# Kernel optimization log

Hardware: AMD Instinct MI355X
Metric: run time of the kernel (lower is better)

Reference implementation:

```python
import jax, jax.numpy as jnp
import numpy as np

DELTA = 0.1  # fixed Gaussian temperature from __init__


def setup_inputs() -> dict:
    key = jax.random.key(0)
    k1, k2 = jax.random.split(key)
    B, T_TEXT, C = 16, 1024, 512
    T_FEAT = 4096  # static upper bound on sum(durations) per row (durations < 5 -> max 4*1024)
    x = jax.random.normal(k1, (B, T_TEXT, C), dtype=jnp.float32)
    durations = jax.random.randint(k2, (B, T_TEXT), 0, 5, dtype=jnp.int32)
    text_mask = jnp.ones((B, T_TEXT), dtype=bool)  # seqs_layout: valid text positions
    return {"x": x, "durations": durations, "text_mask": text_mask, "t_feat": T_FEAT}


def reference(x, durations, text_mask, t_feat):
    # x: (B, T_text, C); durations: (B, T_text) int; text_mask: (B, T_text) bool
    dtype = x.dtype
    d = durations.astype(dtype)
    out_lens = d.sum(axis=1)                                   # (B,)
    t = jnp.arange(t_feat, dtype=dtype)[None, :]               # (1, T_feat)
    y_mask = t < out_lens[:, None]                             # (B, T_feat) valid frames
    t = t * y_mask.astype(dtype)                               # zero out padded frames
    c = jnp.cumsum(d, axis=-1) - d * 0.5                       # (B, T_text) token centers
    # Gaussian energy over (frame, token) pairs: (B, T_feat, T_text)
    energy = -DELTA * (t[:, :, None] - c[:, None, :]) ** 2
    energy = jnp.where(text_mask[:, None, :], energy, -jnp.inf)
    p_attn = jax.nn.softmax(energy, axis=2)                    # softmax over T_text
    y = jnp.einsum("bft,btc->bfc", p_attn, x)                  # (B, T_feat, C)
    return y, out_lens.astype(jnp.int32)
```

## Files before the change

kernel.cpp:

```cpp
#include <hip/hip_runtime.h>
#include <stdint.h>


#define T_TEXT 1024
#define NEGK -0.14426950408889634f
#define CUT 6.5f
#define WIN2F 49.0f

typedef float vfloat4 __attribute__((ext_vector_type(4)));

__device__ __forceinline__ void nt_store4(float* p, float4 v) {
    vfloat4 nv;
    nv.x = v.x; nv.y = v.y; nv.z = v.z; nv.w = v.w;
    __builtin_nontemporal_store(nv, (vfloat4*)p);
}

#define FMA_GROUP(W4, XV)                                                    \
    {                                                                        \
        const float4 w4 = W4;                                                \
        const float ws = (w4.x + w4.y) + (w4.z + w4.w);                      \
        if (ws != 0.f) {                                                     \
            acc[f].x += w4.x * XV[0].x; acc[f].y += w4.x * XV[0].y;          \
            acc[f].z += w4.x * XV[0].z; acc[f].w += w4.x * XV[0].w;          \
            acc[f].x += w4.y * XV[1].x; acc[f].y += w4.y * XV[1].y;          \
            acc[f].z += w4.y * XV[1].z; acc[f].w += w4.y * XV[1].w;          \
            acc[f].x += w4.z * XV[2].x; acc[f].y += w4.z * XV[2].y;          \
            acc[f].z += w4.z * XV[2].z; acc[f].w += w4.z * XV[2].w;          \
            acc[f].x += w4.w * XV[3].x; acc[f].y += w4.w * XV[3].y;          \
            acc[f].z += w4.w * XV[3].z; acc[f].w += w4.w * XV[3].w;          \
            den[f] += ws;                                                    \
        }                                                                    \
    }

__global__ __launch_bounds__(256, 4) void gauss_kernel(const float* __restrict__ x,
                                                       const int* __restrict__ dur,
                                                       float* __restrict__ y,
                                                       float* __restrict__ out_lens_f,
                                                       int F) {
    const int C = 512;
    int bid = blockIdx.x;
    const int nwg = gridDim.x;
    if ((nwg & 7) == 0) bid = (bid & 7) * (nwg >> 3) + (bid >> 3);
    const int nt = F >> 4;
    const int b = bid / nt;
    const int f0 = (bid - b * nt) << 4;
    const int tid = threadIdx.x;
    const int lane = tid & 63, wid = tid >> 6;
    const int fg = tid >> 7;
    const int chb = (tid & 127) << 2;

    __shared__ float clds[T_TEXT];
    __shared__ float wlds[16][64];
    __shared__ int wtot[4];
    __shared__ int wred[4];

    const int4 d4 = ((const int4*)(dur + b * T_TEXT))[tid];
    const int p0 = d4.x, p1 = p0 + d4.y, p2 = p1 + d4.z, p3 = p2 + d4.w;
    int s = p3;
#pragma unroll
    for (int off = 1; off < 64; off <<= 1) {
        int n = __shfl_up(s, off);
        if (lane >= off) s += n;
    }
    if (lane == 63) wtot[wid] = s;
    __syncthreads();
    int base = s - p3;
    const int w0 = wtot[0], w1 = wtot[1], w2 = wtot[2], w3 = wtot[3];
    const int out_len = (w0 + w1) + (w2 + w3);
    if (wid > 0) base += w0;
    if (wid > 1) base += w1;
    if (wid > 2) base += w2;
    float4 cv;
    cv.x = (float)(base + p0) - 0.5f * (float)d4.x;
    cv.y = (float)(base + p1) - 0.5f * (float)d4.y;
    cv.z = (float)(base + p2) - 0.5f * (float)d4.z;
    cv.w = (float)(base + p3) - 0.5f * (float)d4.w;
    *(float4*)&clds[tid << 2] = cv;

    const float wlo = (float)f0 - CUT;
    const float whi = (float)(f0 + 15) + CUT;
    const int cl = (cv.x < wlo) + (cv.y < wlo) + (cv.z < wlo) + (cv.w < wlo);
    const int ch = (cv.x <= whi) + (cv.y <= whi) + (cv.z <= whi) + (cv.w <= whi);
    const int cc = (cv.x <= CUT) + (cv.y <= CUT) + (cv.z <= CUT) + (cv.w <= CUT);
    int pack = cl | (ch << 10) | (cc << 20);
#pragma unroll
    for (int off = 1; off < 64; off <<= 1) pack += __shfl_xor(pack, off);
    if (lane == 0) wred[wid] = pack;
    __syncthreads();

    const int r0 = wred[0], r1 = wred[1], r2 = wred[2], r3 = wred[3];
    int jlo = (r0 & 1023) + (r1 & 1023) + (r2 & 1023) + (r3 & 1023);
    const int jhi = ((r0 >> 10) & 1023) + ((r1 >> 10) & 1023) +
                    ((r2 >> 10) & 1023) + ((r3 >> 10) & 1023);
    const int jhi0 = ((r0 >> 20) & 1023) + ((r1 >> 20) & 1023) +
                     ((r2 >> 20) & 1023) + ((r3 >> 20) & 1023);

    if (f0 == 0 && tid == 0) out_lens_f[b] = (float)out_len;

    int nvalid = out_len - f0;
    nvalid = nvalid < 0 ? 0 : (nvalid > 16 ? 16 : nvalid);

    const float* xb = x + (size_t)b * T_TEXT * C + chb;
    float* yb = y + ((size_t)b * F + f0) * C + chb;

    if (nvalid < 16) {
        float4 a = make_float4(0.f, 0.f, 0.f, 0.f);
        float dn = 0.f;
        for (int j = 0; j < jhi0; j += 4) {
            const float4 c4 = *(const float4*)&clds[j];
            float w[4];
            w[0] = (j + 0 < jhi0) ? exp2f(NEGK * c4.x * c4.x) : 0.f;
            w[1] = (j + 1 < jhi0) ? exp2f(NEGK * c4.y * c4.y) : 0.f;
            w[2] = (j + 2 < jhi0) ? exp2f(NEGK * c4.z * c4.z) : 0.f;
            w[3] = (j + 3 < jhi0) ? exp2f(NEGK * c4.w * c4.w) : 0.f;
            float4 xv[4];
#pragma unroll
            for (int q = 0; q < 4; ++q) {
                int jj = j + q;
                jj = jj < T_TEXT ? jj : T_TEXT - 1;
                xv[q] = *(const float4*)&xb[(size_t)jj * C];
            }
#pragma unroll
            for (int q = 0; q < 4; ++q) {
                a.x += w[q] * xv[q].x; a.y += w[q] * xv[q].y;
                a.z += w[q] * xv[q].z; a.w += w[q] * xv[q].w;
                dn += w[q];
            }
        }
        const float inv = 1.0f / dn;
        const float4 r = make_float4(a.x * inv, a.y * inv, a.z * inv, a.w * inv);
        for (int row = nvalid + fg; row < 16; row += 2)
            nt_store4(&yb[(size_t)row * C], r);
    }

    if (nvalid > 0) {
        float4 acc[8];
        float den[8];
#pragma unroll
        for (int i = 0; i < 8; ++i) { acc[i] = make_float4(0.f, 0.f, 0.f, 0.f); den[i] = 0.f; }

        jlo &= ~3;

        bool first = true;
        for (int j0 = jlo; j0 < jhi; j0 += 64) {
            if (!first) __syncthreads();
            {
                const int f = tid >> 4;
                const int tq = (tid & 15) << 2;
                const int j = j0 + tq;
                const float tf = (f < nvalid) ? (float)(f0 + f) : -3000.0f;
                float4 w4 = make_float4(0.f, 0.f, 0.f, 0.f);
                if (j < T_TEXT) {
                    const float4 c4 = *(const float4*)&clds[j];
                    const float e0 = tf - c4.x, e1 = tf - c4.y, e2 = tf - c4.z, e3 = tf - c4.w;
                    const float s0 = e0 * e0, s1 = e1 * e1, s2 = e2 * e2, s3 = e3 * e3;
                    if (j + 0 < jhi && s0 <= WIN2F) w4.x = exp2f(NEGK * s0);
                    if (j + 1 < jhi && s1 <= WIN2F) w4.y = exp2f(NEGK * s1);
                    if (j + 2 < jhi && s2 <= WIN2F) w4.z = exp2f(NEGK * s2);
                    if (j + 3 < jhi && s3 <= WIN2F) w4.w = exp2f(NEGK * s3);
                }
                *(float4*)&wlds[f][tq] = w4;
            }
            __syncthreads();
            first = false;

            int ntok = jhi - j0;
            if (ntok > 64) ntok = 64;
            for (int g = 0; g < ntok; g += 4) {
                float4 xv[4];
#pragma unroll
                for (int q = 0; q < 4; ++q) {
                    int jj = j0 + g + q;
                    jj = jj < T_TEXT ? jj : T_TEXT - 1;
                    xv[q] = *(const float4*)&xb[(size_t)jj * C];
                }
#pragma unroll
                for (int f = 0; f < 8; ++f) FMA_GROUP((*(const float4*)&wlds[fg * 8 + f][g]), xv);
            }
        }
#pragma unroll
        for (int f = 0; f < 8; ++f) {
            const int row = fg * 8 + f;
            if (row < nvalid) {
                const float inv = 1.0f / den[f];
                nt_store4(&yb[(size_t)row * C],
                          make_float4(acc[f].x * inv, acc[f].y * inv, acc[f].z * inv, acc[f].w * inv));
            }
        }
    }
}

extern "C" void kernel_launch(void* const* d_in, const int* in_sizes, int n_in,
                              void* d_out, int out_size, void* d_ws, size_t ws_size,
                              hipStream_t stream) {
    const float* x = (const float*)d_in[0];
    const int* dur = (const int*)d_in[1];

    const int B = in_sizes[1] / T_TEXT;
    const int C = in_sizes[0] / in_sizes[1];
    const int F = (out_size / B - 1) / C;

    float* yout = (float*)d_out;
    float* out_lens_f = yout + (size_t)B * F * C;

    gauss_kernel<<<B * (F / 16), 256, 0, stream>>>(x, dur, yout, out_lens_f, F);
}
```

Baseline: 33.81 us.

## Process two frame tiles per workgroup, pairing low and high halves

Each workgroup now handles two 16-frame tiles, one from the first half of F and one from the second half, which halves the grid size. The per-row duration prefix scan and center computation are amortized over two tiles. Because valid frames cluster at low indices, this also pairs busy tiles with mostly padded ones to balance load. The cost is fewer workgroups, which may reduce latency hiding and parallelism on a GPU with many CUs.

Result: no change. 33.52 us (-0.9%).

```diff
diff --git a/kernel.cpp b/kernel.cpp
--- a/kernel.cpp
+++ b/kernel.cpp
@@ -41,9 +41,11 @@
     int bid = blockIdx.x;
     const int nwg = gridDim.x;
     if ((nwg & 7) == 0) bid = (bid & 7) * (nwg >> 3) + (bid >> 3);
-    const int nt = F >> 4;
-    const int b = bid / nt;
-    const int f0 = (bid - b * nt) << 4;
+    const int npair = F >> 5;
+    const int b = bid / npair;
+    const int tp = bid - b * npair;
+    const int f0a = tp << 4;
+    const int f0b = f0a + (F >> 1);
     const int tid = threadIdx.x;
     const int lane = tid & 63, wid = tid >> 6;
     const int fg = tid >> 7;
@@ -52,7 +54,8 @@
     __shared__ float clds[T_TEXT];
     __shared__ float wlds[16][64];
     __shared__ int wtot[4];
-    __shared__ int wred[4];
+    __shared__ int wredA[4];
+    __shared__ int wredB[4];
 
     const int4 d4 = ((const int4*)(dur + b * T_TEXT))[tid];
     const int p0 = d4.x, p1 = p0 + d4.y, p2 = p1 + d4.z, p3 = p2 + d4.w;
@@ -77,33 +80,39 @@
     cv.w = (float)(base + p3) - 0.5f * (float)d4.w;
     *(float4*)&clds[tid << 2] = cv;
 
-    const float wlo = (float)f0 - CUT;
-    const float whi = (float)(f0 + 15) + CUT;
-    const int cl = (cv.x < wlo) + (cv.y < wlo) + (cv.z < wlo) + (cv.w < wlo);
-    const int ch = (cv.x <= whi) + (cv.y <= whi) + (cv.z <= whi) + (cv.w <= whi);
-    const int cc = (cv.x <= CUT) + (cv.y <= CUT) + (cv.z <= CUT) + (cv.w <= CUT);
-    int pack = cl | (ch << 10) | (cc << 20);
-#pragma unroll
-    for (int off = 1; off < 64; off <<= 1) pack += __shfl_xor(pack, off);
-    if (lane == 0) wred[wid] = pack;
+    const float wloa = (float)f0a - CUT, whia = (float)(f0a + 15) + CUT;
+    const float wlob = (float)f0b - CUT, whib = (float)(f0b + 15) + CUT;
+    int pa = ((cv.x < wloa) + (cv.y < wloa) + (cv.z < wloa) + (cv.w < wloa))
+           | (((cv.x <= whia) + (cv.y <= whia) + (cv.z <= whia) + (cv.w <= whia)) << 10)
+           | (((cv.x <= CUT) + (cv.y <= CUT) + (cv.z <= CUT) + (cv.w <= CUT)) << 20);
+    int pb = ((cv.x < wlob) + (cv.y < wlob) + (cv.z < wlob) + (cv.w < wlob))
+           | (((cv.x <= whib) + (cv.y <= whib) + (cv.z <= whib) + (cv.w <= whib)) << 10);
+#pragma unroll
+    for (int off = 1; off < 64; off <<= 1) {
+        pa += __shfl_xor(pa, off);
+        pb += __shfl_xor(pb, off);
+    }
+    if (lane == 0) { wredA[wid] = pa; wredB[wid] = pb; }
     __syncthreads();
 
-    const int r0 = wred[0], r1 = wred[1], r2 = wred[2], r3 = wred[3];
-    int jlo = (r0 & 1023) + (r1 & 1023) + (r2 & 1023) + (r3 & 1023);
-    const int jhi = ((r0 >> 10) & 1023) + ((r1 >> 10) & 1023) +
-                    ((r2 >> 10) & 1023) + ((r3 >> 10) & 1023);
-    const int jhi0 = ((r0 >> 20) & 1023) + ((r1 >> 20) & 1023) +
-                     ((r2 >> 20) & 1023) + ((r3 >> 20) & 1023);
-
-    if (f0 == 0 && tid == 0) out_lens_f[b] = (float)out_len;
-
-    int nvalid = out_len - f0;
-    nvalid = nvalid < 0 ? 0 : (nvalid > 16 ? 16 : nvalid);
+    int jloa = 0, jhia = 0, jhi0 = 0, jlob = 0, jhib = 0;
+#pragma unroll
+    for (int w = 0; w < 4; ++w) {
+        const int ra = wredA[w], rb = wredB[w];
+        jloa += ra & 1023; jhia += (ra >> 10) & 1023; jhi0 += (ra >> 20) & 1023;
+        jlob += rb & 1023; jhib += (rb >> 10) & 1023;
+    }
+
+    if (tp == 0 && tid == 0) out_lens_f[b] = (float)out_len;
+
+    int nva = out_len - f0a; nva = nva < 0 ? 0 : (nva > 16 ? 16 : nva);
+    int nvb = out_len - f0b; nvb = nvb < 0 ? 0 : (nvb > 16 ? 16 : nvb);
 
     const float* xb = x + (size_t)b * T_TEXT * C + chb;
-    float* yb = y + ((size_t)b * F + f0) * C + chb;
-
-    if (nvalid < 16) {
+    float* yba = y + ((size_t)b * F + f0a) * C + chb;
+    float* ybb = y + ((size_t)b * F + f0b) * C + chb;
+
+    if (nva < 16 || nvb < 16) {
         float4 a = make_float4(0.f, 0.f, 0.f, 0.f);
         float dn = 0.f;
         for (int j = 0; j < jhi0; j += 4) {
@@ -129,26 +138,34 @@
         }
         const float inv = 1.0f / dn;
         const float4 r = make_float4(a.x * inv, a.y * inv, a.z * inv, a.w * inv);
-        for (int row = nvalid + fg; row < 16; row += 2)
-            nt_store4(&yb[(size_t)row * C], r);
-    }
-
-    if (nvalid > 0) {
+        for (int row = nva + fg; row < 16; row += 2)
+            nt_store4(&yba[(size_t)row * C], r);
+        for (int row = nvb + fg; row < 16; row += 2)
+            nt_store4(&ybb[(size_t)row * C], r);
+    }
+
+    bool need_bar = false;
+#pragma unroll
+    for (int tt = 0; tt < 2; ++tt) {
+        const int nv = tt ? nvb : nva;
+        if (nv <= 0) continue;
+        const int f0 = tt ? f0b : f0a;
+        const int jhi = tt ? jhib : jhia;
+        int jlo = (tt ? jlob : jloa) & ~3;
+        float* yb = tt ? ybb : yba;
+
         float4 acc[8];
         float den[8];
 #pragma unroll
         for (int i = 0; i < 8; ++i) { acc[i] = make_float4(0.f, 0.f, 0.f, 0.f); den[i] = 0.f; }
 
-        jlo &= ~3;
-
-        bool first = true;
         for (int j0 = jlo; j0 < jhi; j0 += 64) {
-            if (!first) __syncthreads();
+            if (need_bar) __syncthreads();
             {
                 const int f = tid >> 4;
                 const int tq = (tid & 15) << 2;
                 const int j = j0 + tq;
-                const float tf = (f < nvalid) ? (float)(f0 + f) : -3000.0f;
+                const float tf = (f < nv) ? (float)(f0 + f) : -3000.0f;
                 float4 w4 = make_float4(0.f, 0.f, 0.f, 0.f);
                 if (j < T_TEXT) {
                     const float4 c4 = *(const float4*)&clds[j];
@@ -162,7 +179,7 @@
                 *(float4*)&wlds[f][tq] = w4;
             }
             __syncthreads();
-            first = false;
+            need_bar = true;
 
             int ntok = jhi - j0;
             if (ntok > 64) ntok = 64;
@@ -181,7 +198,7 @@
 #pragma unroll
         for (int f = 0; f < 8; ++f) {
             const int row = fg * 8 + f;
-            if (row < nvalid) {
+            if (row < nv) {
                 const float inv = 1.0f / den[f];
                 nt_store4(&yb[(size_t)row * C],
                           make_float4(acc[f].x * inv, acc[f].y * inv, acc[f].z * inv, acc[f].w * inv));
@@ -203,5 +220,5 @@
     float* yout = (float*)d_out;
     float* out_lens_f = yout + (size_t)B * F * C;
 
-    gauss_kernel<<<B * (F / 16), 256, 0, stream>>>(x, dur, yout, out_lens_f, F);
+    gauss_kernel<<<B * (F >> 5), 256, 0, stream>>>(x, dur, yout, out_lens_f, F);
 }
```
